# Performance work log

Measured on AMD Instinct MI355X. Metric: run time of the kernel, lower is better.

The kernel has to match this reference:

```python
import jax, jax.numpy as jnp
import numpy as np

# Model dims (match init_kwargs / input_specs)
L, D, H, F = 4, 1024, 16, 4096   # layers, d_model, heads, ffn hidden
B, S = 4, 1024                    # batch, seq_len
HD = D // H                       # head dim = 64
K = 8                             # context-mask band width (k=8, 2//k == 0)
LN_EPS = 1e-5


def setup_inputs():
    key = jax.random.key(0)
    ks = jax.random.split(key, 16)
    s = 0.02  # init scale for weights
    return {
        "src":   jax.random.normal(ks[0], (B, S, D), jnp.float32),
        # stacked per-layer params (leading dim L)
        "Wqkv":  jax.random.normal(ks[1], (L, 3 * D, D), jnp.float32) * s,
        "bqkv":  jnp.zeros((L, 3 * D), jnp.float32),
        "Wo":    jax.random.normal(ks[2], (L, D, D), jnp.float32) * s,
        "bo":    jnp.zeros((L, D), jnp.float32),
        "W1":    jax.random.normal(ks[3], (L, F, D), jnp.float32) * s,
        "b1":    jnp.zeros((L, F), jnp.float32),
        "W2":    jax.random.normal(ks[4], (L, D, F), jnp.float32) * s,
        "b2":    jnp.zeros((L, D), jnp.float32),
        "ln1_w": jnp.ones((L, D), jnp.float32),
        "ln1_b": jnp.zeros((L, D), jnp.float32),
        "ln2_w": jnp.ones((L, D), jnp.float32),
        "ln2_b": jnp.zeros((L, D), jnp.float32),
    }


def _layer_norm(x, g, b):
    m = jnp.mean(x, axis=-1, keepdims=True)
    v = jnp.mean(jnp.square(x - m), axis=-1, keepdims=True)
    return (x - m) * jax.lax.rsqrt(v + LN_EPS) * g + b


def _context_mask(sz):
    # row i allows keys j with i <= j < i + K (clamped into range); 0 allowed, -inf masked
    i = jnp.arange(sz)[:, None]
    j = jnp.arange(sz)[None, :]
    return jnp.where((j >= i) & (j < i + K), 0.0, -jnp.inf).astype(jnp.float32)


def reference(src, Wqkv, bqkv, Wo, bo, W1, b1, W2, b2, ln1_w, ln1_b, ln2_w, ln2_b):
    mask = _context_mask(S)  # [S, S] additive mask
    scale = 1.0 / jnp.sqrt(jnp.float32(HD))
    x = src  # [B, S, D] (batch-first; equivalent to torch's permute round-trip)
    for l in range(L):
        # --- self-attention (post-norm, dropout=0) ---
        qkv = jnp.einsum('bsd,ed->bse', x, Wqkv[l]) + bqkv[l]  # [B,S,3D]
        q, k, v = jnp.split(qkv, 3, axis=-1)
        q = q.reshape(B, S, H, HD).transpose(0, 2, 1, 3)  # [B,H,S,HD]
        k = k.reshape(B, S, H, HD).transpose(0, 2, 1, 3)
        v = v.reshape(B, S, H, HD).transpose(0, 2, 1, 3)
        scores = jnp.einsum('bhqd,bhkd->bhqk', q, k) * scale + mask
        attn = jax.nn.softmax(scores, axis=-1)
        o = jnp.einsum('bhqk,bhkd->bhqd', attn, v)
        o = o.transpose(0, 2, 1, 3).reshape(B, S, D)
        o = jnp.einsum('bsd,ed->bse', o, Wo[l]) + bo[l]
        x = _layer_norm(x + o, ln1_w[l], ln1_b[l])
        # --- feed-forward, exact (erf) gelu ---
        h = jax.nn.gelu(jnp.einsum('bsd,fd->bsf', x, W1[l]) + b1[l], approximate=False)
        h = jnp.einsum('bsf,df->bsd', h, W2[l]) + b2[l]
        x = _layer_norm(x + h, ln2_w[l], ln2_b[l])
    return x
```

## Files before the change

kernel.cpp:

```cpp
#include <hip/hip_runtime.h>

#define LNUM 4
#define DMODEL 1024
#define NHEAD 16
#define FDIM 4096
#define BATCH 4
#define SEQ 1024
#define HDIM 64
#define KBAND 8
#define MROWS (BATCH * SEQ)

typedef __attribute__((ext_vector_type(8))) __bf16 bf16x8;
typedef __attribute__((ext_vector_type(4))) float f32x4;
typedef __attribute__((ext_vector_type(8))) unsigned short u16x8;

__device__ __forceinline__ unsigned short f2bf(float f) {
  unsigned int u = __builtin_bit_cast(unsigned int, f);
  u = u + 0x7fffu + ((u >> 16) & 1u);
  return (unsigned short)(u >> 16);
}
__device__ __forceinline__ float bf2f(unsigned short h) {
  unsigned int u = ((unsigned int)h) << 16;
  return __builtin_bit_cast(float, u);
}

#define GLOAD16(gp, lp)                                                        \
  __builtin_amdgcn_global_load_lds(                                            \
      (const __attribute__((address_space(1))) void*)(gp),                     \
      (__attribute__((address_space(3))) void*)(lp), 16, 0, 0)

__global__ __launch_bounds__(256) void cvt_bf16(const float* __restrict__ in,
                                                unsigned short* __restrict__ out,
                                                long n) {
  long i = ((long)blockIdx.x * 256 + threadIdx.x) * 4;
  if (i + 3 < n) {
    float4 v = *reinterpret_cast<const float4*>(in + i);
    ushort4 o;
    o.x = f2bf(v.x);
    o.y = f2bf(v.y);
    o.z = f2bf(v.z);
    o.w = f2bf(v.w);
    *reinterpret_cast<ushort4*>(out + i) = o;
  }
}

template <int EPI>
__global__ __launch_bounds__(256, 3) void gemm128(const unsigned short* __restrict__ A,
                                                  const unsigned short* __restrict__ W,
                                                  const float* __restrict__ bias,
                                                  unsigned short* __restrict__ Cout,
                                                  int Ndim, int Kdim, int Ks) {
  __shared__ unsigned short SH[8192];
  unsigned short* As = SH;
  unsigned short* Bs = SH + 4096;
  const int tid = threadIdx.x;
  const int wave = tid >> 6;
  const int lane = tid & 63;

  const int gx = gridDim.x, gy = gridDim.y;
  const int nwg = gx * gy;
  const int lin = blockIdx.x + blockIdx.y * gx;
  const int q8 = nwg >> 3, r8 = nwg & 7;
  const int xcd = lin & 7, cidx = lin >> 3;
  const int cbase = (xcd < r8) ? xcd * (q8 + 1) : r8 * (q8 + 1) + (xcd - r8) * q8;
  const int swz = cbase + cidx;
  const int bm0 = (swz % gy) * 128;
  const int bn0 = (swz / gy) * 128;
  const int kz0 = blockIdx.z * Ks;

  const int r0 = tid >> 2;
  const int c0 = (((tid & 3) ^ ((tid >> 3) & 3)) << 3);
  const unsigned short* gA = A + (size_t)(bm0 + r0) * Kdim + kz0 + c0;
  const unsigned short* gB = W + (size_t)(bn0 + r0) * Kdim + kz0 + c0;
  const size_t rowstep = (size_t)64 * Kdim;

  f32x4 acc[4][4] = {};

  const int wr = (wave >> 1) * 64;
  const int wc = (wave & 1) * 64;
  const int fr = lane & 15;
  const int kg = lane >> 4;
  const int kofs = ((kg ^ ((fr >> 1) & 3)) << 3);

  const int nt = Ks >> 5;
  for (int t = 0; t < nt; ++t) {
    GLOAD16(gA, &As[wave * 512]);
    GLOAD16(gA + rowstep, &As[2048 + wave * 512]);
    GLOAD16(gB, &Bs[wave * 512]);
    GLOAD16(gB + rowstep, &Bs[2048 + wave * 512]);
    gA += 32;
    gB += 32;
    __syncthreads();
    bf16x8 af[4], bfr[4];
#pragma unroll
    for (int i = 0; i < 4; ++i)
      af[i] = *reinterpret_cast<const bf16x8*>(&As[(wr + i * 16 + fr) * 32 + kofs]);
#pragma unroll
    for (int j = 0; j < 4; ++j)
      bfr[j] = *reinterpret_cast<const bf16x8*>(&Bs[(wc + j * 16 + fr) * 32 + kofs]);
#pragma unroll
    for (int i = 0; i < 4; ++i)
#pragma unroll
      for (int j = 0; j < 4; ++j)
        acc[i][j] = __builtin_amdgcn_mfma_f32_16x16x32_bf16(af[i], bfr[j], acc[i][j], 0, 0, 0);
    __syncthreads();
  }

  const int rr = (lane >> 4) * 4;
  const int cc = lane & 15;
  const bool addb = (EPI != 2) || (blockIdx.z == 0);
  unsigned short* outZ =
      Cout + (EPI == 2 ? (size_t)blockIdx.z * ((size_t)gy * 128) * Ndim : 0);
  float bv[4];
#pragma unroll
  for (int j = 0; j < 4; ++j)
    bv[j] = addb ? bias[bn0 + wc + j * 16 + cc] : 0.0f;

  unsigned short* lt = SH + wave * 1280;
#pragma unroll
  for (int rh = 0; rh < 2; ++rh) {
#pragma unroll
    for (int cp = 0; cp < 2; ++cp) {
#pragma unroll
      for (int ii = 0; ii < 2; ++ii)
#pragma unroll
        for (int jj = 0; jj < 2; ++jj)
#pragma unroll
          for (int r = 0; r < 4; ++r) {
            float v = acc[rh * 2 + ii][cp * 2 + jj][r] + bv[cp * 2 + jj];
            if (EPI == 1) v = 0.5f * v * (1.0f + erff(v * 0.70710678118654752f));
            lt[(ii * 16 + rr + r) * 40 + jj * 16 + cc] = f2bf(v);
          }
      asm volatile("s_waitcnt lgkmcnt(0)" ::: "memory");
      const int rl = lane >> 1;
      const int chalf = (lane & 1) * 16;
      u16x8 o0 = *reinterpret_cast<const u16x8*>(&lt[rl * 40 + chalf]);
      u16x8 o1 = *reinterpret_cast<const u16x8*>(&lt[rl * 40 + chalf + 8]);
      const int m = bm0 + wr + rh * 32 + rl;
      const int n0 = bn0 + wc + cp * 32 + chalf;
      unsigned short* dst = outZ + (size_t)m * Ndim + n0;
      *reinterpret_cast<u16x8*>(dst) = o0;
      *reinterpret_cast<u16x8*>(dst + 8) = o1;
      asm volatile("s_waitcnt lgkmcnt(0)" ::: "memory");
    }
  }
}

__global__ __launch_bounds__(256) void attn_band(const unsigned short* __restrict__ qkv,
                                                 unsigned short* __restrict__ outp) {
  const int gw = blockIdx.x * 4 + (threadIdx.x >> 6);
  const int lane = threadIdx.x & 63;
  const int q = gw & (SEQ - 1);
  const int bh = gw >> 10;
  const int h = bh & (NHEAD - 1);
  const int b = bh >> 4;
  const size_t row0 = (size_t)(b * SEQ + q);
  const size_t stride = 3 * DMODEL;
  const float qv = bf2f(qkv[row0 * stride + h * HDIM + lane]);

  float sc[KBAND];
  float mx = -1e30f;
#pragma unroll
  for (int jj = 0; jj < KBAND; ++jj) {
    const int j = q + jj;
    const int jc = (j < SEQ) ? j : (SEQ - 1);
    float kv = bf2f(qkv[(size_t)(b * SEQ + jc) * stride + DMODEL + h * HDIM + lane]);
    float p = qv * kv;
#pragma unroll
    for (int m = 32; m; m >>= 1) p += __shfl_xor(p, m);
    p *= 0.125f;
    p = (j < SEQ) ? p : -1e30f;
    sc[jj] = p;
    mx = fmaxf(mx, p);
  }
  float denom = 0.f;
  float ov = 0.f;
#pragma unroll
  for (int jj = 0; jj < KBAND; ++jj) {
    const int j = q + jj;
    const int jc = (j < SEQ) ? j : (SEQ - 1);
    float p = __expf(sc[jj] - mx);
    p = (j < SEQ) ? p : 0.f;
    denom += p;
    ov += p * bf2f(qkv[(size_t)(b * SEQ + jc) * stride + 2 * DMODEL + h * HDIM + lane]);
  }
  ov /= denom;
  outp[row0 * DMODEL + h * HDIM + lane] = f2bf(ov);
}

__global__ __launch_bounds__(256) void add_ln2(const float* __restrict__ resid,
                                               const unsigned short* __restrict__ part,
                                               const float* __restrict__ gw,
                                               const float* __restrict__ gb,
                                               float* __restrict__ xf,
                                               unsigned short* __restrict__ xb) {
  const int row = blockIdx.x;
  const int tid = threadIdx.x;
  const size_t slab = (size_t)MROWS * DMODEL;
  const float* rp = resid + (size_t)row * DMODEL;
  const unsigned short* pp = part + (size_t)row * DMODEL;
  float v[4];
  float s = 0.f, s2 = 0.f;
#pragma unroll
  for (int i = 0; i < 4; ++i) {
    const int idx = tid + i * 256;
    float a = rp[idx] + bf2f(pp[idx]) + bf2f(pp[slab + idx]);
    v[i] = a;
    s += a;
    s2 += a * a;
  }
#pragma unroll
  for (int m = 32; m; m >>= 1) {
    s += __shfl_xor(s, m);
    s2 += __shfl_xor(s2, m);
  }
  __shared__ float wsm[8];
  const int wave = tid >> 6, lane = tid & 63;
  if (lane == 0) {
    wsm[wave] = s;
    wsm[4 + wave] = s2;
  }
  __syncthreads();
  s = wsm[0] + wsm[1] + wsm[2] + wsm[3];
  s2 = wsm[4] + wsm[5] + wsm[6] + wsm[7];
  const float mean = s * (1.f / DMODEL);
  const float var = s2 * (1.f / DMODEL) - mean * mean;
  const float rstd = rsqrtf(var + 1e-5f);
#pragma unroll
  for (int i = 0; i < 4; ++i) {
    const int idx = tid + i * 256;
    const float y = (v[i] - mean) * rstd * gw[idx] + gb[idx];
    xf[(size_t)row * DMODEL + idx] = y;
    xb[(size_t)row * DMODEL + idx] = f2bf(y);
  }
}

extern "C" void kernel_launch(void* const* d_in, const int* in_sizes, int n_in,
                              void* d_out, int out_size, void* d_ws, size_t ws_size,
                              hipStream_t stream) {
  const float* src  = (const float*)d_in[0];
  const float* Wqkv = (const float*)d_in[1];
  const float* bqkv = (const float*)d_in[2];
  const float* Wo   = (const float*)d_in[3];
  const float* bo   = (const float*)d_in[4];
  const float* W1   = (const float*)d_in[5];
  const float* b1   = (const float*)d_in[6];
  const float* W2   = (const float*)d_in[7];
  const float* b2   = (const float*)d_in[8];
  const float* ln1w = (const float*)d_in[9];
  const float* ln1b = (const float*)d_in[10];
  const float* ln2w = (const float*)d_in[11];
  const float* ln2b = (const float*)d_in[12];
  float* out = (float*)d_out;

  char* p = (char*)d_ws;
  unsigned short* wqkv_b = (unsigned short*)p; p += (size_t)LNUM * 3072 * 1024 * 2;
  unsigned short* wo_b   = (unsigned short*)p; p += (size_t)LNUM * 1024 * 1024 * 2;
  unsigned short* w1_b   = (unsigned short*)p; p += (size_t)LNUM * 4096 * 1024 * 2;
  unsigned short* w2_b   = (unsigned short*)p; p += (size_t)LNUM * 1024 * 4096 * 2;
  float*          xf     = (float*)p;          p += (size_t)MROWS * DMODEL * 4;
  unsigned short* xb     = (unsigned short*)p; p += (size_t)MROWS * DMODEL * 2;
  char* R = p;
  unsigned short* qkvb = (unsigned short*)R;
  unsigned short* aob  = (unsigned short*)(R + (size_t)MROWS * 3 * DMODEL * 2);
  unsigned short* hb   = (unsigned short*)R;
  unsigned short* part = (unsigned short*)(R + (size_t)MROWS * 4096 * 2);
  p = R + (size_t)MROWS * 4096 * 2 + (size_t)2 * MROWS * DMODEL * 2;
  if (ws_size < (size_t)(p - (char*)d_ws)) return;

  cvt_bf16<<<(long)LNUM * 3072 * 1024 / 1024, 256, 0, stream>>>(Wqkv, wqkv_b, (long)LNUM * 3072 * 1024);
  cvt_bf16<<<(long)LNUM * 1024 * 1024 / 1024, 256, 0, stream>>>(Wo, wo_b, (long)LNUM * 1024 * 1024);
  cvt_bf16<<<(long)LNUM * 4096 * 1024 / 1024, 256, 0, stream>>>(W1, w1_b, (long)LNUM * 4096 * 1024);
  cvt_bf16<<<(long)LNUM * 1024 * 4096 / 1024, 256, 0, stream>>>(W2, w2_b, (long)LNUM * 1024 * 4096);
  cvt_bf16<<<(long)MROWS * DMODEL / 1024, 256, 0, stream>>>(src, xb, (long)MROWS * DMODEL);

  for (int l = 0; l < LNUM; ++l) {
    gemm128<0><<<dim3(3072 / 128, MROWS / 128, 1), 256, 0, stream>>>(
        xb, wqkv_b + (size_t)l * 3072 * 1024, bqkv + l * 3072, qkvb, 3072, 1024, 1024);
    attn_band<<<(BATCH * NHEAD * SEQ) / 4, 256, 0, stream>>>(qkvb, aob);
    gemm128<2><<<dim3(1024 / 128, MROWS / 128, 2), 256, 0, stream>>>(
        aob, wo_b + (size_t)l * 1024 * 1024, bo + l * 1024, part, 1024, 1024, 512);
    add_ln2<<<MROWS, 256, 0, stream>>>(l == 0 ? src : xf, part,
                                       ln1w + l * DMODEL, ln1b + l * DMODEL, xf, xb);
    gemm128<1><<<dim3(FDIM / 128, MROWS / 128, 1), 256, 0, stream>>>(
        xb, w1_b + (size_t)l * 4096 * 1024, b1 + l * FDIM, hb, FDIM, 1024, 1024);
    gemm128<2><<<dim3(1024 / 128, MROWS / 128, 2), 256, 0, stream>>>(
        hb, w2_b + (size_t)l * 1024 * 4096, b2 + l * 1024, part, 1024, 4096, 2048);
    float* dst = (l == LNUM - 1) ? out : xf;
    add_ln2<<<MROWS, 256, 0, stream>>>(xf, part,
                                       ln2w + l * DMODEL, ln2b + l * DMODEL, dst, xb);
  }
}
```

Before: 942.5 us.

## Double-buffer GEMM LDS tiles and raise FFN2 split-K to four

The GEMM main loop now prefetches the next K-tile into a second LDS buffer while MFMAs run on the current one. It uses explicit vmcnt waits and raw barriers instead of a load-then-sync on every iteration. Separately, the W2 GEMM is split over four K-slices instead of two, and the add+layernorm kernel takes a slice count to sum the partials. This trades doubled LDS per block, which may lower occupancy, and extra partial-buffer traffic for better latency hiding and more blocks on the long-K GEMM.

```diff
diff --git a/kernel.cpp b/kernel.cpp
--- a/kernel.cpp
+++ b/kernel.cpp
@@ -50,9 +50,7 @@
                                                   const float* __restrict__ bias,
                                                   unsigned short* __restrict__ Cout,
                                                   int Ndim, int Kdim, int Ks) {
-  __shared__ unsigned short SH[8192];
-  unsigned short* As = SH;
-  unsigned short* Bs = SH + 4096;
+  __shared__ unsigned short SH[16384];
   const int tid = threadIdx.x;
   const int wave = tid >> 6;
   const int lane = tid & 63;
@@ -82,15 +80,32 @@
   const int kg = lane >> 4;
   const int kofs = ((kg ^ ((fr >> 1) & 3)) << 3);
 
+#define STAGE(buf, kt)                                                         \
+  do {                                                                         \
+    const unsigned short* pa = gA + (size_t)(kt) * 32;                         \
+    const unsigned short* pb = gB + (size_t)(kt) * 32;                         \
+    unsigned short* la = &SH[(buf) * 8192];                                    \
+    unsigned short* lb = &SH[(buf) * 8192 + 4096];                             \
+    GLOAD16(pa, la + wave * 512);                                              \
+    GLOAD16(pa + rowstep, la + 2048 + wave * 512);                             \
+    GLOAD16(pb, lb + wave * 512);                                              \
+    GLOAD16(pb + rowstep, lb + 2048 + wave * 512);                             \
+  } while (0)
+
   const int nt = Ks >> 5;
+  STAGE(0, 0);
   for (int t = 0; t < nt; ++t) {
-    GLOAD16(gA, &As[wave * 512]);
-    GLOAD16(gA + rowstep, &As[2048 + wave * 512]);
-    GLOAD16(gB, &Bs[wave * 512]);
-    GLOAD16(gB + rowstep, &Bs[2048 + wave * 512]);
-    gA += 32;
-    gB += 32;
-    __syncthreads();
+    const int cur = t & 1;
+    if (t + 1 < nt) {
+      STAGE(cur ^ 1, t + 1);
+      asm volatile("s_waitcnt vmcnt(4)" ::: "memory");
+    } else {
+      asm volatile("s_waitcnt vmcnt(0)" ::: "memory");
+    }
+    __builtin_amdgcn_s_barrier();
+    asm volatile("" ::: "memory");
+    const unsigned short* As = &SH[cur * 8192];
+    const unsigned short* Bs = &SH[cur * 8192 + 4096];
     bf16x8 af[4], bfr[4];
 #pragma unroll
     for (int i = 0; i < 4; ++i)
@@ -103,8 +118,10 @@
 #pragma unroll
       for (int j = 0; j < 4; ++j)
         acc[i][j] = __builtin_amdgcn_mfma_f32_16x16x32_bf16(af[i], bfr[j], acc[i][j], 0, 0, 0);
-    __syncthreads();
-  }
+    asm volatile("" ::: "memory");
+    __builtin_amdgcn_s_barrier();
+  }
+#undef STAGE
 
   const int rr = (lane >> 4) * 4;
   const int cc = lane & 15;
@@ -188,12 +205,13 @@
   outp[row0 * DMODEL + h * HDIM + lane] = f2bf(ov);
 }
 
-__global__ __launch_bounds__(256) void add_ln2(const float* __restrict__ resid,
-                                               const unsigned short* __restrict__ part,
-                                               const float* __restrict__ gw,
-                                               const float* __restrict__ gb,
-                                               float* __restrict__ xf,
-                                               unsigned short* __restrict__ xb) {
+__global__ __launch_bounds__(256) void add_ln(const float* __restrict__ resid,
+                                              const unsigned short* __restrict__ part,
+                                              int nz,
+                                              const float* __restrict__ gw,
+                                              const float* __restrict__ gb,
+                                              float* __restrict__ xf,
+                                              unsigned short* __restrict__ xb) {
   const int row = blockIdx.x;
   const int tid = threadIdx.x;
   const size_t slab = (size_t)MROWS * DMODEL;
@@ -204,7 +222,8 @@
 #pragma unroll
   for (int i = 0; i < 4; ++i) {
     const int idx = tid + i * 256;
-    float a = rp[idx] + bf2f(pp[idx]) + bf2f(pp[slab + idx]);
+    float a = rp[idx];
+    for (int z = 0; z < nz; ++z) a += bf2f(pp[z * slab + idx]);
     v[i] = a;
     s += a;
     s2 += a * a;
@@ -265,7 +284,7 @@
   unsigned short* aob  = (unsigned short*)(R + (size_t)MROWS * 3 * DMODEL * 2);
   unsigned short* hb   = (unsigned short*)R;
   unsigned short* part = (unsigned short*)(R + (size_t)MROWS * 4096 * 2);
-  p = R + (size_t)MROWS * 4096 * 2 + (size_t)2 * MROWS * DMODEL * 2;
+  p = R + (size_t)MROWS * 4096 * 2 + (size_t)4 * MROWS * DMODEL * 2;
   if (ws_size < (size_t)(p - (char*)d_ws)) return;
 
   cvt_bf16<<<(long)LNUM * 3072 * 1024 / 1024, 256, 0, stream>>>(Wqkv, wqkv_b, (long)LNUM * 3072 * 1024);
@@ -280,14 +299,14 @@
     attn_band<<<(BATCH * NHEAD * SEQ) / 4, 256, 0, stream>>>(qkvb, aob);
     gemm128<2><<<dim3(1024 / 128, MROWS / 128, 2), 256, 0, stream>>>(
         aob, wo_b + (size_t)l * 1024 * 1024, bo + l * 1024, part, 1024, 1024, 512);
-    add_ln2<<<MROWS, 256, 0, stream>>>(l == 0 ? src : xf, part,
-                                       ln1w + l * DMODEL, ln1b + l * DMODEL, xf, xb);
+    add_ln<<<MROWS, 256, 0, stream>>>(l == 0 ? src : xf, part, 2,
+                                      ln1w + l * DMODEL, ln1b + l * DMODEL, xf, xb);
     gemm128<1><<<dim3(FDIM / 128, MROWS / 128, 1), 256, 0, stream>>>(
         xb, w1_b + (size_t)l * 4096 * 1024, b1 + l * FDIM, hb, FDIM, 1024, 1024);
-    gemm128<2><<<dim3(1024 / 128, MROWS / 128, 2), 256, 0, stream>>>(
-        hb, w2_b + (size_t)l * 1024 * 4096, b2 + l * 1024, part, 1024, 4096, 2048);
+    gemm128<2><<<dim3(1024 / 128, MROWS / 128, 4), 256, 0, stream>>>(
+        hb, w2_b + (size_t)l * 1024 * 4096, b2 + l * 1024, part, 1024, 4096, 1024);
     float* dst = (l == LNUM - 1) ? out : xf;
-    add_ln2<<<MROWS, 256, 0, stream>>>(xf, part,
-                                       ln2w + l * DMODEL, ln2b + l * DMODEL, dst, xb);
-  }
-}
+    add_ln<<<MROWS, 256, 0, stream>>>(xf, part, 4,
+                                      ln2w + l * DMODEL, ln2b + l * DMODEL, dst, xb);
+  }
+}
```

Measured after the change: 1.009 ms. 7.0% more time.
